# Kernel tuning notes

Measured on AMD Instinct MI355X. Metric: run time of the kernel, lower is better.

Reference implementation:

```python
import jax, jax.numpy as jnp
import numpy as np

BITS = 4
GROUPSIZE = 128
INF = 4096
OUTF = 11008
MAXQ = (1 << BITS) - 1  # 15
NGROUPS = INF // GROUPSIZE  # 32
NTOK = 256


def setup_inputs() -> dict:
    key = jax.random.key(0)
    k0, k1, k2, k3, k4 = jax.random.split(key, 5)
    imin = jnp.iinfo(jnp.int32).min
    imax = jnp.iinfo(jnp.int32).max
    x = jax.random.normal(k0, (NTOK, INF), dtype=jnp.float32)
    qweight = jax.random.randint(k1, (INF // 32 * BITS, OUTF), imin, imax, dtype=jnp.int32)
    qzeros = jax.random.randint(k2, (NGROUPS, OUTF // 32 * BITS), imin, imax, dtype=jnp.int32)
    # per-group scales: small positive values, realistic for 4-bit quant
    scales = jax.random.uniform(k3, (NGROUPS, OUTF), dtype=jnp.float32, minval=1e-3, maxval=1e-2)
    bias = jax.random.normal(k4, (OUTF,), dtype=jnp.float32)
    g_idx = (jnp.arange(INF) // GROUPSIZE).astype(jnp.int32)
    return {"x": x, "scales": scales, "bias": bias,
            "qweight": qweight, "qzeros": qzeros, "g_idx": g_idx}


def reference(x, scales, bias, qweight, qzeros, g_idx):
    # bit offsets within each packed int32 word: [0,4,8,...,28]
    wf = jnp.arange(0, 32, BITS, dtype=jnp.int32)  # [8]

    # unpack zeros: [G, OUTF//8] int32 -> [G, OUTF//8, 8] -> [G, OUTF]
    zeros = ((qzeros[:, :, None] >> wf[None, None, :]) & MAXQ) + 1
    zeros = zeros.reshape(scales.shape)  # [G, OUTF]

    # unpack weights: [INF//8, OUTF] int32 -> [INF//8, 8, OUTF] -> [INF, OUTF]
    weight = (qweight[:, None, :] >> wf[None, :, None]) & MAXQ
    weight = weight.reshape(-1, qweight.shape[1])  # [INF, OUTF]

    # group-wise dequant: w[i, o] = scales[g_idx[i], o] * (q[i, o] - zeros[g_idx[i], o])
    w = scales[g_idx] * (weight.astype(scales.dtype) - zeros[g_idx].astype(scales.dtype))

    out = jnp.matmul(x, w) + bias  # [NTOK, OUTF]
    return out
```

## Files before the change

### kernel.cpp

```cpp
#include <hip/hip_runtime.h>
#include <stdint.h>

#define INF    4096
#define OUTF   11008
#define NTOK   256
#define QZ_COLS (OUTF / 8)
#define NTILES  (INF / 128)

#define BM 64
#define BN 64

typedef __attribute__((ext_vector_type(8))) _Float16 f16x8;
typedef __attribute__((ext_vector_type(2))) _Float16 f16x2;
typedef __attribute__((ext_vector_type(4))) float    f32x4;

static_assert(sizeof(f16x8) == 16, "f16x8 must be 16B");

__global__ __launch_bounds__(256, 2)
void qlin_mfma(const float* __restrict__ x,
               const float* __restrict__ scales,
               const float* __restrict__ bias,
               const int*   __restrict__ qweight,
               const int*   __restrict__ qzeros,
               float*       __restrict__ out)
{
    __shared__ uint32_t A_sh[16][BM][4];
    __shared__ uint32_t B_sh[16][BN][4];

    const int tid = threadIdx.x;
    const int n0  = blockIdx.x * BN;
    const int m0  = blockIdx.y * BM;

    const int lane = tid & 63;
    const int wid  = tid >> 6;
    const int wm   = wid >> 1;
    const int wn   = wid & 1;
    const int l15  = lane & 15;
    const int l4   = lane >> 4;

    float acc[2][2][4];
    f32x4 accg[2][2];
    #pragma unroll
    for (int i = 0; i < 2; ++i)
        #pragma unroll
        for (int j = 0; j < 2; ++j) {
            accg[i][j] = f32x4{0.f, 0.f, 0.f, 0.f};
            #pragma unroll
            for (int r = 0; r < 4; ++r) acc[i][j][r] = 0.f;
        }

    const int oL  = tid & 63;
    const int thi = tid >> 6;
    const int zsh = (oL & 7) * 4;
    const int zwordIdx = (n0 + oL) >> 3;

    const int a_kc = tid & 15;
    const int a_m  = tid >> 4;

    for (int t = 0; t < NTILES; ++t) {
        float sj[2];
        #pragma unroll
        for (int j = 0; j < 2; ++j)
            sj[j] = scales[t * OUTF + n0 + wn * 32 + j * 16 + l15];

        const int zw = qzeros[t * QZ_COLS + zwordIdx];
        const int z  = ((zw >> zsh) & 15) + 1;
        const _Float16 hz = (_Float16)(float)(1024 + z);
        const f16x2 z2 = {hz, hz};

        #pragma unroll
        for (int r = 0; r < 4; ++r) {
            const int m = a_m + r * 16;
            const float* src = x + (size_t)(m0 + m) * INF + t * 128 + a_kc * 8;
            const f32x4 v0 = *(const f32x4*)src;
            const f32x4 v1 = *(const f32x4*)(src + 4);
            uint32_t d[4];
            #pragma unroll
            for (int p = 0; p < 4; ++p)
                d[p] = __builtin_bit_cast(uint32_t,
                          __builtin_amdgcn_cvt_pkrtz(v0[p], v1[p]));
            *(uint4*)&A_sh[a_kc][(m) ^ (a_kc & 7)][0] = make_uint4(d[0], d[1], d[2], d[3]);
        }

        #pragma unroll
        for (int r = 0; r < 4; ++r) {
            const int k8 = r * 4 + thi;
            const uint32_t w = (uint32_t)qweight[(size_t)(t * 16 + k8) * OUTF + n0 + oL];
            uint32_t d[4];
            #pragma unroll
            for (int p = 0; p < 4; ++p) {
                const uint32_t bv = ((w >> (4 * p)) & 0x000F000Fu) | 0x64006400u;
                const f16x2 hv = __builtin_bit_cast(f16x2, bv) - z2;
                d[p] = __builtin_bit_cast(uint32_t, hv);
            }
            *(uint4*)&B_sh[k8][oL][0] = make_uint4(d[0], d[1], d[2], d[3]);
        }

        __syncthreads();

        #pragma unroll
        for (int kk = 0; kk < 4; ++kk) {
            const int k8 = kk * 4 + l4;
            f16x8 a[2], b[2];
            #pragma unroll
            for (int i = 0; i < 2; ++i)
                a[i] = *(const f16x8*)&A_sh[k8][(wm * 32 + i * 16 + l15) ^ (k8 & 7)][0];
            #pragma unroll
            for (int j = 0; j < 2; ++j)
                b[j] = *(const f16x8*)&B_sh[k8][wn * 32 + j * 16 + l15][0];
            #pragma unroll
            for (int i = 0; i < 2; ++i)
                #pragma unroll
                for (int j = 0; j < 2; ++j)
                    accg[i][j] = __builtin_amdgcn_mfma_f32_16x16x32_f16(
                                     a[i], b[j], accg[i][j], 0, 0, 0);
        }

        #pragma unroll
        for (int j = 0; j < 2; ++j)
            #pragma unroll
            for (int i = 0; i < 2; ++i) {
                #pragma unroll
                for (int r = 0; r < 4; ++r) {
                    acc[i][j][r] += sj[j] * accg[i][j][r];
                }
                accg[i][j] = f32x4{0.f, 0.f, 0.f, 0.f};
            }

        __syncthreads();
    }

    #pragma unroll
    for (int j = 0; j < 2; ++j) {
        const int col = n0 + wn * 32 + j * 16 + l15;
        const float bv = bias[col];
        #pragma unroll
        for (int i = 0; i < 2; ++i) {
            const int row0 = m0 + wm * 32 + i * 16 + l4 * 4;
            #pragma unroll
            for (int r = 0; r < 4; ++r)
                out[(size_t)(row0 + r) * OUTF + col] = acc[i][j][r] + bv;
        }
    }
}

extern "C" void kernel_launch(void* const* d_in, const int* in_sizes, int n_in,
                              void* d_out, int out_size, void* d_ws, size_t ws_size,
                              hipStream_t stream)
{
    const float* x       = (const float*)d_in[0];
    const float* scales  = (const float*)d_in[1];
    const float* bias    = (const float*)d_in[2];
    const int*   qweight = (const int*)d_in[3];
    const int*   qzeros  = (const int*)d_in[4];
    float* out = (float*)d_out;

    dim3 grid(OUTF / BN, NTOK / BM);
    qlin_mfma<<<grid, dim3(256), 0, stream>>>(x, scales, bias, qweight, qzeros, out);
}
```

Measured before the change: 133.9 us.

## Prefetch next tile's global loads into registers during MFMA compute

Moves the global loads of x, qweight, qzeros and scales for tile t+1 into registers, issuing them after the first barrier so they overlap the MFMA loop of tile t. The main loop then only converts and stores already-loaded registers to shared memory. This hides global memory latency at the cost of about 40 more VGPRs per thread, which could reduce occupancy under launch_bounds(256,2). The last iteration issues a redundant reload of the final tile.

```diff
diff --git a/kernel.cpp b/kernel.cpp
--- a/kernel.cpp
+++ b/kernel.cpp
@@ -57,46 +57,58 @@
     const int a_kc = tid & 15;
     const int a_m  = tid >> 4;
 
+    f32x4    pv0[4], pv1[4];
+    uint32_t pw[4];
+    int      pzw;
+    float    psj0, psj1;
+
+    auto issue = [&](int t) {
+        #pragma unroll
+        for (int r = 0; r < 4; ++r) {
+            const float* src = x + (size_t)(m0 + a_m + r * 16) * INF + t * 128 + a_kc * 8;
+            pv0[r] = *(const f32x4*)src;
+            pv1[r] = *(const f32x4*)(src + 4);
+        }
+        #pragma unroll
+        for (int r = 0; r < 4; ++r)
+            pw[r] = (uint32_t)qweight[(size_t)(t * 16 + r * 4 + thi) * OUTF + n0 + oL];
+        pzw  = qzeros[t * QZ_COLS + zwordIdx];
+        psj0 = scales[t * OUTF + n0 + wn * 32 + l15];
+        psj1 = scales[t * OUTF + n0 + wn * 32 + 16 + l15];
+    };
+
+    issue(0);
+
     for (int t = 0; t < NTILES; ++t) {
-        float sj[2];
-        #pragma unroll
-        for (int j = 0; j < 2; ++j)
-            sj[j] = scales[t * OUTF + n0 + wn * 32 + j * 16 + l15];
-
-        const int zw = qzeros[t * QZ_COLS + zwordIdx];
-        const int z  = ((zw >> zsh) & 15) + 1;
+        const int z = ((pzw >> zsh) & 15) + 1;
         const _Float16 hz = (_Float16)(float)(1024 + z);
         const f16x2 z2 = {hz, hz};
+        const float sjf0 = psj0, sjf1 = psj1;
 
         #pragma unroll
         for (int r = 0; r < 4; ++r) {
-            const int m = a_m + r * 16;
-            const float* src = x + (size_t)(m0 + m) * INF + t * 128 + a_kc * 8;
-            const f32x4 v0 = *(const f32x4*)src;
-            const f32x4 v1 = *(const f32x4*)(src + 4);
             uint32_t d[4];
             #pragma unroll
             for (int p = 0; p < 4; ++p)
                 d[p] = __builtin_bit_cast(uint32_t,
-                          __builtin_amdgcn_cvt_pkrtz(v0[p], v1[p]));
-            *(uint4*)&A_sh[a_kc][(m) ^ (a_kc & 7)][0] = make_uint4(d[0], d[1], d[2], d[3]);
+                          __builtin_amdgcn_cvt_pkrtz(pv0[r][p], pv1[r][p]));
+            *(uint4*)&A_sh[a_kc][(a_m + r * 16) ^ (a_kc & 7)][0] =
+                make_uint4(d[0], d[1], d[2], d[3]);
         }
-
         #pragma unroll
         for (int r = 0; r < 4; ++r) {
-            const int k8 = r * 4 + thi;
-            const uint32_t w = (uint32_t)qweight[(size_t)(t * 16 + k8) * OUTF + n0 + oL];
             uint32_t d[4];
             #pragma unroll
             for (int p = 0; p < 4; ++p) {
-                const uint32_t bv = ((w >> (4 * p)) & 0x000F000Fu) | 0x64006400u;
-                const f16x2 hv = __builtin_bit_cast(f16x2, bv) - z2;
-                d[p] = __builtin_bit_cast(uint32_t, hv);
+                const uint32_t bv = ((pw[r] >> (4 * p)) & 0x000F000Fu) | 0x64006400u;
+                d[p] = __builtin_bit_cast(uint32_t, __builtin_bit_cast(f16x2, bv) - z2);
             }
-            *(uint4*)&B_sh[k8][oL][0] = make_uint4(d[0], d[1], d[2], d[3]);
+            *(uint4*)&B_sh[r * 4 + thi][oL][0] = make_uint4(d[0], d[1], d[2], d[3]);
         }
 
         __syncthreads();
+
+        issue((t + 1 < NTILES) ? (t + 1) : (NTILES - 1));
 
         #pragma unroll
         for (int kk = 0; kk < 4; ++kk) {
@@ -117,15 +129,15 @@
         }
 
         #pragma unroll
-        for (int j = 0; j < 2; ++j)
+        for (int i = 0; i < 2; ++i) {
             #pragma unroll
-            for (int i = 0; i < 2; ++i) {
-                #pragma unroll
-                for (int r = 0; r < 4; ++r) {
-                    acc[i][j][r] += sj[j] * accg[i][j][r];
-                }
-                accg[i][j] = f32x4{0.f, 0.f, 0.f, 0.f};
+            for (int r = 0; r < 4; ++r) {
+                acc[i][0][r] += sjf0 * accg[i][0][r];
+                acc[i][1][r] += sjf1 * accg[i][1][r];
             }
+            accg[i][0] = f32x4{0.f, 0.f, 0.f, 0.f};
+            accg[i][1] = f32x4{0.f, 0.f, 0.f, 0.f};
+        }
 
         __syncthreads();
     }
```

Result: faster. 127.4 us (-4.8%).

## Double-buffer LDS tiles and prefetch global loads two tiles ahead

Applied to the files above, without the earlier changes.

Replaces the single-buffered loop with ping-pong LDS buffers and two register sets of prefetched x, qweight, qzeros and scales values, issued two K-tiles ahead. Global loads now overlap the MFMA compute of the current tile. Each tile synchronizes with one lightweight barrier (an LDS waitcnt plus s_barrier) instead of two __syncthreads. In exchange, LDS use doubles and register pressure rises from the held prefetch sets, which may hurt occupancy under launch_bounds(256,2).

```diff
diff --git a/kernel.cpp b/kernel.cpp
--- a/kernel.cpp
+++ b/kernel.cpp
@@ -14,7 +14,67 @@
 typedef __attribute__((ext_vector_type(2))) _Float16 f16x2;
 typedef __attribute__((ext_vector_type(4))) float    f32x4;
 
-static_assert(sizeof(f16x8) == 16, "f16x8 must be 16B");
+#define BAR() do { \
+    asm volatile("s_waitcnt lgkmcnt(0)" ::: "memory"); \
+    __builtin_amdgcn_s_barrier(); \
+} while (0)
+
+#define DECL_SET(S) \
+    f32x4 pv0##S[4], pv1##S[4]; uint32_t pw##S[4]; int pzw##S; float psj0##S, psj1##S;
+
+#define ISSUE(S, T) do { \
+    const int _t = (T); \
+    _Pragma("unroll") for (int r = 0; r < 4; ++r) { \
+        const float* _src = x + (size_t)(m0 + a_m + r * 16) * INF + _t * 128 + a_kc * 8; \
+        pv0##S[r] = *(const f32x4*)_src; \
+        pv1##S[r] = *(const f32x4*)(_src + 4); } \
+    _Pragma("unroll") for (int r = 0; r < 4; ++r) \
+        pw##S[r] = (uint32_t)qweight[(size_t)(_t * 16 + r * 4 + thi) * OUTF + n0 + oL]; \
+    pzw##S  = qzeros[_t * QZ_COLS + zwordIdx]; \
+    psj0##S = scales[_t * OUTF + n0 + wn * 32 + l15]; \
+    psj1##S = scales[_t * OUTF + n0 + wn * 32 + 16 + l15]; \
+} while (0)
+
+#define DEQUANT(S, BUF) do { \
+    const int _z = ((pzw##S >> zsh) & 15) + 1; \
+    const _Float16 _hz = (_Float16)(float)(1024 + _z); \
+    const f16x2 _z2 = {_hz, _hz}; \
+    _Pragma("unroll") for (int r = 0; r < 4; ++r) { \
+        uint32_t d[4]; \
+        _Pragma("unroll") for (int p = 0; p < 4; ++p) \
+            d[p] = __builtin_bit_cast(uint32_t, \
+                      __builtin_amdgcn_cvt_pkrtz(pv0##S[r][p], pv1##S[r][p])); \
+        *(uint4*)&A_sh[BUF][a_kc][(a_m + r * 16) ^ (a_kc & 7)][0] = \
+            make_uint4(d[0], d[1], d[2], d[3]); } \
+    _Pragma("unroll") for (int r = 0; r < 4; ++r) { \
+        uint32_t d[4]; \
+        _Pragma("unroll") for (int p = 0; p < 4; ++p) { \
+            const uint32_t bv = ((pw##S[r] >> (4 * p)) & 0x000F000Fu) | 0x64006400u; \
+            d[p] = __builtin_bit_cast(uint32_t, __builtin_bit_cast(f16x2, bv) - _z2); } \
+        *(uint4*)&B_sh[BUF][r * 4 + thi][oL][0] = make_uint4(d[0], d[1], d[2], d[3]); } \
+    cs0_nxt = psj0##S; cs1_nxt = psj1##S; \
+} while (0)
+
+#define COMPUTE(BUF) do { \
+    _Pragma("unroll") for (int kk = 0; kk < 4; ++kk) { \
+        const int k8 = kk * 4 + l4; \
+        f16x8 a[2], b[2]; \
+        _Pragma("unroll") for (int i = 0; i < 2; ++i) \
+            a[i] = *(const f16x8*)&A_sh[BUF][k8][(wm * 32 + i * 16 + l15) ^ (k8 & 7)][0]; \
+        _Pragma("unroll") for (int j = 0; j < 2; ++j) \
+            b[j] = *(const f16x8*)&B_sh[BUF][k8][wn * 32 + j * 16 + l15][0]; \
+        _Pragma("unroll") for (int i = 0; i < 2; ++i) \
+            _Pragma("unroll") for (int j = 0; j < 2; ++j) \
+                accg[i][j] = __builtin_amdgcn_mfma_f32_16x16x32_f16( \
+                                 a[i], b[j], accg[i][j], 0, 0, 0); \
+    } \
+    _Pragma("unroll") for (int i = 0; i < 2; ++i) { \
+        _Pragma("unroll") for (int r = 0; r < 4; ++r) { \
+            acc[i][0][r] += cs0_cur * accg[i][0][r]; \
+            acc[i][1][r] += cs1_cur * accg[i][1][r]; } \
+        accg[i][0] = f32x4{0.f, 0.f, 0.f, 0.f}; \
+        accg[i][1] = f32x4{0.f, 0.f, 0.f, 0.f}; } \
+} while (0)
 
 __global__ __launch_bounds__(256, 2)
 void qlin_mfma(const float* __restrict__ x,
@@ -24,8 +84,8 @@
                const int*   __restrict__ qzeros,
                float*       __restrict__ out)
 {
-    __shared__ uint32_t A_sh[16][BM][4];
-    __shared__ uint32_t B_sh[16][BN][4];
+    __shared__ uint32_t A_sh[2][16][BM][4];
+    __shared__ uint32_t B_sh[2][16][BN][4];
 
     const int tid = threadIdx.x;
     const int n0  = blockIdx.x * BN;
@@ -53,81 +113,32 @@
     const int thi = tid >> 6;
     const int zsh = (oL & 7) * 4;
     const int zwordIdx = (n0 + oL) >> 3;
-
     const int a_kc = tid & 15;
     const int a_m  = tid >> 4;
 
-    for (int t = 0; t < NTILES; ++t) {
-        float sj[2];
-        #pragma unroll
-        for (int j = 0; j < 2; ++j)
-            sj[j] = scales[t * OUTF + n0 + wn * 32 + j * 16 + l15];
+    DECL_SET(A)
+    DECL_SET(B)
+    float cs0_cur, cs1_cur, cs0_nxt, cs1_nxt;
 
-        const int zw = qzeros[t * QZ_COLS + zwordIdx];
-        const int z  = ((zw >> zsh) & 15) + 1;
-        const _Float16 hz = (_Float16)(float)(1024 + z);
-        const f16x2 z2 = {hz, hz};
+    ISSUE(A, 0);
+    DEQUANT(A, 0);
+    ISSUE(B, 1);
+    BAR();
 
-        #pragma unroll
-        for (int r = 0; r < 4; ++r) {
-            const int m = a_m + r * 16;
-            const float* src = x + (size_t)(m0 + m) * INF + t * 128 + a_kc * 8;
-            const f32x4 v0 = *(const f32x4*)src;
-            const f32x4 v1 = *(const f32x4*)(src + 4);
-            uint32_t d[4];
-            #pragma unroll
-            for (int p = 0; p < 4; ++p)
-                d[p] = __builtin_bit_cast(uint32_t,
-                          __builtin_amdgcn_cvt_pkrtz(v0[p], v1[p]));
-            *(uint4*)&A_sh[a_kc][(m) ^ (a_kc & 7)][0] = make_uint4(d[0], d[1], d[2], d[3]);
+    for (int t = 0; t < NTILES; t += 2) {
+        cs0_cur = cs0_nxt; cs1_cur = cs1_nxt;
+        if (t + 2 < NTILES) ISSUE(A, t + 2);
+        COMPUTE(0);
+        DEQUANT(B, 1);
+        BAR();
+
+        cs0_cur = cs0_nxt; cs1_cur = cs1_nxt;
+        if (t + 3 < NTILES) ISSUE(B, t + 3);
+        COMPUTE(1);
+        if (t + 2 < NTILES) {
+            DEQUANT(A, 0);
+            BAR();
         }
-
-        #pragma unroll
-        for (int r = 0; r < 4; ++r) {
-            const int k8 = r * 4 + thi;
-            const uint32_t w = (uint32_t)qweight[(size_t)(t * 16 + k8) * OUTF + n0 + oL];
-            uint32_t d[4];
-            #pragma unroll
-            for (int p = 0; p < 4; ++p) {
-                const uint32_t bv = ((w >> (4 * p)) & 0x000F000Fu) | 0x64006400u;
-                const f16x2 hv = __builtin_bit_cast(f16x2, bv) - z2;
-                d[p] = __builtin_bit_cast(uint32_t, hv);
-            }
-            *(uint4*)&B_sh[k8][oL][0] = make_uint4(d[0], d[1], d[2], d[3]);
-        }
-
-        __syncthreads();
-
-        #pragma unroll
-        for (int kk = 0; kk < 4; ++kk) {
-            const int k8 = kk * 4 + l4;
-            f16x8 a[2], b[2];
-            #pragma unroll
-            for (int i = 0; i < 2; ++i)
-                a[i] = *(const f16x8*)&A_sh[k8][(wm * 32 + i * 16 + l15) ^ (k8 & 7)][0];
-            #pragma unroll
-            for (int j = 0; j < 2; ++j)
-                b[j] = *(const f16x8*)&B_sh[k8][wn * 32 + j * 16 + l15][0];
-            #pragma unroll
-            for (int i = 0; i < 2; ++i)
-                #pragma unroll
-                for (int j = 0; j < 2; ++j)
-                    accg[i][j] = __builtin_amdgcn_mfma_f32_16x16x32_f16(
-                                     a[i], b[j], accg[i][j], 0, 0, 0);
-        }
-
-        #pragma unroll
-        for (int j = 0; j < 2; ++j)
-            #pragma unroll
-            for (int i = 0; i < 2; ++i) {
-                #pragma unroll
-                for (int r = 0; r < 4; ++r) {
-                    acc[i][j][r] += sj[j] * accg[i][j][r];
-                }
-                accg[i][j] = f32x4{0.f, 0.f, 0.f, 0.f};
-            }
-
-        __syncthreads();
     }
 
     #pragma unroll
```

Measured after the change: 150.5 us. 12.4% more time.

## Prepack activations to fp16 and stream them into LDS with direct loads

Applied to the files above, without the earlier changes.

Adds a pre-pass kernel that converts x to fp16 once and writes it in the swizzled tile layout the matmul expects. The main kernel then loads A tiles straight into LDS with global_load_lds instead of converting fp32 in every block. BN drops to 32 and the occupancy hint rises to 6, and scales are folded into the fp16 dequantized weights, which removes the per-tile fp32 rescale of the accumulators. This adds an extra launch and workspace traffic, and fp16 scale multiplication may cost some precision.

```diff
diff --git a/kernel.cpp b/kernel.cpp
--- a/kernel.cpp
+++ b/kernel.cpp
@@ -8,28 +8,52 @@
 #define NTILES  (INF / 128)
 
 #define BM 64
-#define BN 64
+#define BN 32
 
 typedef __attribute__((ext_vector_type(8))) _Float16 f16x8;
 typedef __attribute__((ext_vector_type(2))) _Float16 f16x2;
 typedef __attribute__((ext_vector_type(4))) float    f32x4;
 
-static_assert(sizeof(f16x8) == 16, "f16x8 must be 16B");
+typedef const __attribute__((address_space(1))) uint4 gl_uint4;
+typedef __attribute__((address_space(3)))       uint4 sh_uint4;
 
 __global__ __launch_bounds__(256, 2)
-void qlin_mfma(const float* __restrict__ x,
+void xpack(const float* __restrict__ x, uint4* __restrict__ xw)
+{
+    const int g  = blockIdx.x * 256 + threadIdx.x;
+    const int m  = g >> 9;
+    const int c8 = g & 511;
+    const int t  = c8 >> 4;
+    const int k8 = c8 & 15;
+
+    const float* src = x + (size_t)m * INF + c8 * 8;
+    const f32x4 v0 = *(const f32x4*)src;
+    const f32x4 v1 = *(const f32x4*)(src + 4);
+    uint32_t d[4];
+    #pragma unroll
+    for (int p = 0; p < 4; ++p)
+        d[p] = __builtin_bit_cast(uint32_t, __builtin_amdgcn_cvt_pkrtz(v0[p], v1[p]));
+
+    const int mslot = (m & 63) ^ (k8 & 7);
+    const size_t oi = ((size_t)(m >> 6) * 32 + t) * 1024 + k8 * 64 + mslot;
+    xw[oi] = make_uint4(d[0], d[1], d[2], d[3]);
+}
+
+__global__ __launch_bounds__(256, 6)
+void qlin_mfma(const uint4* __restrict__ xw,
                const float* __restrict__ scales,
                const float* __restrict__ bias,
                const int*   __restrict__ qweight,
                const int*   __restrict__ qzeros,
                float*       __restrict__ out)
 {
-    __shared__ uint32_t A_sh[16][BM][4];
-    __shared__ uint32_t B_sh[16][BN][4];
+    __shared__ uint4 A_sh[16][64];
+    __shared__ uint4 B_sh[16][32];
 
-    const int tid = threadIdx.x;
-    const int n0  = blockIdx.x * BN;
-    const int m0  = blockIdx.y * BM;
+    const int tid   = threadIdx.x;
+    const int n0    = blockIdx.x * BN;
+    const int m_blk = blockIdx.y;
+    const int m0    = m_blk * BM;
 
     const int lane = tid & 63;
     const int wid  = tid >> 6;
@@ -38,109 +62,70 @@
     const int l15  = lane & 15;
     const int l4   = lane >> 4;
 
-    float acc[2][2][4];
-    f32x4 accg[2][2];
-    #pragma unroll
-    for (int i = 0; i < 2; ++i)
-        #pragma unroll
-        for (int j = 0; j < 2; ++j) {
-            accg[i][j] = f32x4{0.f, 0.f, 0.f, 0.f};
-            #pragma unroll
-            for (int r = 0; r < 4; ++r) acc[i][j][r] = 0.f;
-        }
+    f32x4 acc[2] = { f32x4{0.f,0.f,0.f,0.f}, f32x4{0.f,0.f,0.f,0.f} };
 
-    const int oL  = tid & 63;
-    const int thi = tid >> 6;
+    const int oL  = tid & 31;
+    const int bk8 = tid >> 5;
     const int zsh = (oL & 7) * 4;
-    const int zwordIdx = (n0 + oL) >> 3;
+    const int zcol = (n0 + oL) >> 3;
 
-    const int a_kc = tid & 15;
-    const int a_m  = tid >> 4;
+    const uint4* abase = xw + (size_t)m_blk * 32 * 1024;
 
     for (int t = 0; t < NTILES; ++t) {
-        float sj[2];
-        #pragma unroll
-        for (int j = 0; j < 2; ++j)
-            sj[j] = scales[t * OUTF + n0 + wn * 32 + j * 16 + l15];
-
-        const int zw = qzeros[t * QZ_COLS + zwordIdx];
-        const int z  = ((zw >> zsh) & 15) + 1;
-        const _Float16 hz = (_Float16)(float)(1024 + z);
-        const f16x2 z2 = {hz, hz};
+        const uint32_t w0 = (uint32_t)qweight[(size_t)(t * 16 + bk8)     * OUTF + n0 + oL];
+        const uint32_t w1 = (uint32_t)qweight[(size_t)(t * 16 + bk8 + 8) * OUTF + n0 + oL];
+        const int   zw = qzeros[t * QZ_COLS + zcol];
+        const float sf = scales[t * OUTF + n0 + oL];
 
         #pragma unroll
         for (int r = 0; r < 4; ++r) {
-            const int m = a_m + r * 16;
-            const float* src = x + (size_t)(m0 + m) * INF + t * 128 + a_kc * 8;
-            const f32x4 v0 = *(const f32x4*)src;
-            const f32x4 v1 = *(const f32x4*)(src + 4);
-            uint32_t d[4];
-            #pragma unroll
-            for (int p = 0; p < 4; ++p)
-                d[p] = __builtin_bit_cast(uint32_t,
-                          __builtin_amdgcn_cvt_pkrtz(v0[p], v1[p]));
-            *(uint4*)&A_sh[a_kc][(m) ^ (a_kc & 7)][0] = make_uint4(d[0], d[1], d[2], d[3]);
+            const int k8 = wid * 4 + r;
+            const uint4* gp = abase + (size_t)t * 1024 + k8 * 64 + lane;
+            __builtin_amdgcn_global_load_lds((gl_uint4*)gp, (sh_uint4*)&A_sh[k8][0],
+                                             16, 0, 0);
         }
 
+        const int z = ((zw >> zsh) & 15) + 1;
+        const _Float16 hz = (_Float16)(float)(1024 + z);
+        const f16x2 z2 = {hz, hz};
+        const _Float16 hs = (_Float16)sf;
+        const f16x2 s2 = {hs, hs};
+        uint32_t d0[4], d1[4];
         #pragma unroll
-        for (int r = 0; r < 4; ++r) {
-            const int k8 = r * 4 + thi;
-            const uint32_t w = (uint32_t)qweight[(size_t)(t * 16 + k8) * OUTF + n0 + oL];
-            uint32_t d[4];
-            #pragma unroll
-            for (int p = 0; p < 4; ++p) {
-                const uint32_t bv = ((w >> (4 * p)) & 0x000F000Fu) | 0x64006400u;
-                const f16x2 hv = __builtin_bit_cast(f16x2, bv) - z2;
-                d[p] = __builtin_bit_cast(uint32_t, hv);
-            }
-            *(uint4*)&B_sh[k8][oL][0] = make_uint4(d[0], d[1], d[2], d[3]);
+        for (int p = 0; p < 4; ++p) {
+            const uint32_t b0 = ((w0 >> (4 * p)) & 0x000F000Fu) | 0x64006400u;
+            const uint32_t b1 = ((w1 >> (4 * p)) & 0x000F000Fu) | 0x64006400u;
+            d0[p] = __builtin_bit_cast(uint32_t,
+                        (__builtin_bit_cast(f16x2, b0) - z2) * s2);
+            d1[p] = __builtin_bit_cast(uint32_t,
+                        (__builtin_bit_cast(f16x2, b1) - z2) * s2);
         }
+        *(uint4*)&B_sh[bk8][oL]     = make_uint4(d0[0], d0[1], d0[2], d0[3]);
+        *(uint4*)&B_sh[bk8 + 8][oL] = make_uint4(d1[0], d1[1], d1[2], d1[3]);
 
         __syncthreads();
 
         #pragma unroll
         for (int kk = 0; kk < 4; ++kk) {
             const int k8 = kk * 4 + l4;
-            f16x8 a[2], b[2];
-            #pragma unroll
-            for (int i = 0; i < 2; ++i)
-                a[i] = *(const f16x8*)&A_sh[k8][(wm * 32 + i * 16 + l15) ^ (k8 & 7)][0];
-            #pragma unroll
-            for (int j = 0; j < 2; ++j)
-                b[j] = *(const f16x8*)&B_sh[k8][wn * 32 + j * 16 + l15][0];
-            #pragma unroll
-            for (int i = 0; i < 2; ++i)
-                #pragma unroll
-                for (int j = 0; j < 2; ++j)
-                    accg[i][j] = __builtin_amdgcn_mfma_f32_16x16x32_f16(
-                                     a[i], b[j], accg[i][j], 0, 0, 0);
+            const f16x8 a0 = __builtin_bit_cast(f16x8, A_sh[k8][(wm * 32      + l15) ^ (k8 & 7)]);
+            const f16x8 a1 = __builtin_bit_cast(f16x8, A_sh[k8][(wm * 32 + 16 + l15) ^ (k8 & 7)]);
+            const f16x8 b  = __builtin_bit_cast(f16x8, B_sh[k8][wn * 16 + l15]);
+            acc[0] = __builtin_amdgcn_mfma_f32_16x16x32_f16(a0, b, acc[0], 0, 0, 0);
+            acc[1] = __builtin_amdgcn_mfma_f32_16x16x32_f16(a1, b, acc[1], 0, 0, 0);
         }
-
-        #pragma unroll
-        for (int j = 0; j < 2; ++j)
-            #pragma unroll
-            for (int i = 0; i < 2; ++i) {
-                #pragma unroll
-                for (int r = 0; r < 4; ++r) {
-                    acc[i][j][r] += sj[j] * accg[i][j][r];
-                }
-                accg[i][j] = f32x4{0.f, 0.f, 0.f, 0.f};
-            }
 
         __syncthreads();
     }
 
+    const int col = n0 + wn * 16 + l15;
+    const float bv = bias[col];
     #pragma unroll
-    for (int j = 0; j < 2; ++j) {
-        const int col = n0 + wn * 32 + j * 16 + l15;
-        const float bv = bias[col];
+    for (int i = 0; i < 2; ++i) {
+        const int row0 = m0 + wm * 32 + i * 16 + l4 * 4;
         #pragma unroll
-        for (int i = 0; i < 2; ++i) {
-            const int row0 = m0 + wm * 32 + i * 16 + l4 * 4;
-            #pragma unroll
-            for (int r = 0; r < 4; ++r)
-                out[(size_t)(row0 + r) * OUTF + col] = acc[i][j][r] + bv;
-        }
+        for (int r = 0; r < 4; ++r)
+            out[(size_t)(row0 + r) * OUTF + col] = acc[i][r] + bv;
     }
 }
 
@@ -154,7 +139,9 @@
     const int*   qweight = (const int*)d_in[3];
     const int*   qzeros  = (const int*)d_in[4];
     float* out = (float*)d_out;
+    uint4* xw  = (uint4*)d_ws;
 
+    xpack<<<dim3(512), dim3(256), 0, stream>>>(x, xw);
     dim3 grid(OUTF / BN, NTOK / BM);
-    qlin_mfma<<<grid, dim3(256), 0, stream>>>(x, scales, bias, qweight, qzeros, out);
+    qlin_mfma<<<grid, dim3(256), 0, stream>>>(xw, scales, bias, qweight, qzeros, out);
 }
```

Measured after the change: 131.8 us. No clear change (-1.6%).
